# Performance work log

Hardware: AMD Instinct MI355X
Metric: run time of the kernel (lower is better)

The kernel has to match this reference:

```python
import jax, jax.numpy as jnp
import numpy as np

B, NV = 8, 2048
HALF_ANGLE = 20.0  # degrees
EXPDEL = 4.0


def to_circle(x):
    # cast angle (rad) to [-pi, pi)
    return jnp.remainder(x + jnp.pi, 2.0 * jnp.pi) - jnp.pi


def setup_inputs() -> dict:
    key = jax.random.key(0)
    k1, k2 = jax.random.split(key)
    raw = jax.random.normal(k1, (B, NV, 5), dtype=jnp.float32)
    # per-feature scaling: x, y ~ 200 m spread; v ~ N(10, 8) m/s; psi ~ N(0, pi); psidot small
    scale = jnp.array([200.0, 200.0, 8.0, np.pi, 0.1], dtype=jnp.float32)
    offset = jnp.array([0.0, 0.0, 10.0, 0.0, 0.0], dtype=jnp.float32)
    state = (raw * scale + offset).reshape(B, NV * 5)
    lengths = 4.0 + 2.0 * jax.random.uniform(k2, (NV,), dtype=jnp.float32)
    return {
        "state": state,
        "lengths": lengths,
        "v0": jnp.array([11.17], dtype=jnp.float32),
        "s0": jnp.array([3.0], dtype=jnp.float32),
        "dth": jnp.array([5.0], dtype=jnp.float32),
        "amax": jnp.array([1.5], dtype=jnp.float32),
        "b": jnp.array([4.0], dtype=jnp.float32),
    }


def reference(state, lengths, v0, s0, dth, amax, b):
    lead_dims = state.shape[:-1]
    s = state.reshape(lead_dims + (-1, 5))
    nv = s.shape[-2]
    x, y, v, psi = s[..., 0], s[..., 1], s[..., 2], s[..., 3]  # [..., nv]

    # pairwise: axis -2 = candidate i, axis -1 = ego j  (dx[i, j] = x_i - x_j)
    dx = x[..., :, None] - x[..., None, :]
    dy = y[..., :, None] - y[..., None, :]
    dr = jnp.sqrt(dx * dx + dy * dy)
    delpsi = to_circle(jnp.arctan2(dy, dx) - psi[..., None, :])  # bearing of i rel. to ego j heading
    ndist = dr * jnp.cos(delpsi)  # longitudinal distance along ego heading

    cone = (ndist > 0) & (jnp.abs(delpsi) < HALF_ANGLE * jnp.pi / 180.0)
    ndist_ = jnp.where(cone, ndist, jnp.inf)
    cndist = jnp.min(ndist_, axis=-2)       # [..., nv] nearest in-cone distance per ego
    inds = jnp.argmin(ndist_, axis=-2)      # [..., nv] index of leading vehicle

    vx = v * jnp.cos(psi)
    vy = v * jnp.sin(psi)
    dvx = jnp.take_along_axis(vx, inds, axis=-1) - vx
    dvy = jnp.take_along_axis(vy, inds, axis=-1) - vy
    dv = jnp.sqrt(dvx * dvx + dvy * dvy)
    vdelpsi = to_circle(jnp.arctan2(dvy, dvx) - psi)
    ndv = dv * jnp.cos(vdelpsi)

    sstar = s0 + v * dth + v * ndv / (2.0 * jnp.sqrt(amax * b))
    sal = cndist - lengths  # ego length subtracted (as in source)
    finite = jnp.isfinite(sal)
    sal_safe = jnp.where(finite, sal, 1.0)  # avoids inf in discarded branch

    action_free = amax * (1.0 - (v / v0) ** EXPDEL)
    action_int = -amax * (sstar / sal_safe) ** 2
    action = jnp.where(finite, action_free + action_int, action_free)
    return action[..., None]  # [..., nv, 1] to match torch output shape
```

## Files before the change

### kernel.cpp

```cpp
#include <hip/hip_runtime.h>
#include <math.h>

namespace {
constexpr int NVEH = 2048;
constexpr int THREADS = 256;
constexpr int EGOS_PER_WAVE = 4;
constexpr int WAVES = THREADS / 64;
constexpr int EGOS_PER_BLOCK = WAVES * EGOS_PER_WAVE;
constexpr int BLOCKS_PER_BATCH = NVEH / EGOS_PER_BLOCK;
}

__global__ __launch_bounds__(THREADS, 4) void idm_kernel(
    const float* __restrict__ state,
    const float* __restrict__ lengths,
    const float* __restrict__ v0p, const float* __restrict__ s0p,
    const float* __restrict__ dthp, const float* __restrict__ amaxp,
    const float* __restrict__ bp,
    float* __restrict__ out)
{
    __shared__ float2 sxy[NVEH];

    const int b = blockIdx.x / BLOCKS_PER_BATCH;
    const int egoBase = (blockIdx.x % BLOCKS_PER_BATCH) * EGOS_PER_BLOCK;
    const float* __restrict__ st = state + (size_t)b * NVEH * 5;

    for (int i = threadIdx.x; i < NVEH; i += THREADS) {
        sxy[i] = make_float2(st[i * 5 + 0], st[i * 5 + 1]);
    }
    __syncthreads();

    const int wave = threadIdx.x >> 6;
    const int lane = threadIdx.x & 63;
    const int j0 = egoBase + wave * EGOS_PER_WAVE;

    float xj[EGOS_PER_WAVE], yj[EGOS_PER_WAVE], vj[EGOS_PER_WAVE];
    float cp[EGOS_PER_WAVE], sp[EGOS_PER_WAVE];
    #pragma unroll
    for (int e = 0; e < EGOS_PER_WAVE; e++) {
        const int j = j0 + e;
        xj[e] = st[j * 5 + 0];
        yj[e] = st[j * 5 + 1];
        vj[e] = st[j * 5 + 2];
        float psi = st[j * 5 + 3];
        float s, c;
        sincosf(psi, &s, &c);
        cp[e] = c; sp[e] = s;
    }

    const float chalf = 0.93969262078590838f;
    const float c2 = chalf * chalf;

    float minv[EGOS_PER_WAVE];
    int   mini[EGOS_PER_WAVE];
    #pragma unroll
    for (int e = 0; e < EGOS_PER_WAVE; e++) { minv[e] = INFINITY; mini[e] = 0; }

    for (int k = 0; k < NVEH / 64; k++) {
        const int i = k * 64 + lane;
        const float2 xy = sxy[i];
        #pragma unroll
        for (int e = 0; e < EGOS_PER_WAVE; e++) {
            const float dx = xy.x - xj[e];
            const float dy = xy.y - yj[e];
            const float proj = dx * cp[e] + dy * sp[e];
            const float dr2 = dx * dx + dy * dy;
            const bool cone = (proj > 0.0f) && (proj * proj > dr2 * c2);
            if (cone && (proj < minv[e])) {
                minv[e] = proj;
                mini[e] = i;
            }
        }
    }

    #pragma unroll
    for (int e = 0; e < EGOS_PER_WAVE; e++) {
        float v = minv[e];
        int idx = mini[e];
        #pragma unroll
        for (int off = 32; off > 0; off >>= 1) {
            const float ov = __shfl_xor(v, off, 64);
            const int oi = __shfl_xor(idx, off, 64);
            if (ov < v || (ov == v && oi < idx)) { v = ov; idx = oi; }
        }
        minv[e] = v;
        mini[e] = idx;
    }

    if (lane == 0) {
        const float v0v = *v0p;
        const float s0v = *s0p;
        const float dthv = *dthp;
        const float am = *amaxp;
        const float bv = *bp;
        const float inv2sab = 1.0f / (2.0f * sqrtf(am * bv));

        #pragma unroll
        for (int e = 0; e < EGOS_PER_WAVE; e++) {
            const int j = j0 + e;
            const float vE = vj[e];
            const float t = vE / v0v;
            const float t2 = t * t;
            const float action_free = am * (1.0f - t2 * t2);
            float action = action_free;

            const float cnd = minv[e];
            if (cnd < 1.0e30f) {
                const int ind = mini[e];
                const float vl = st[ind * 5 + 2];
                const float pl = st[ind * 5 + 3];
                float sl, cl;
                sincosf(pl, &sl, &cl);
                const float dvx = vl * cl - vE * cp[e];
                const float dvy = vl * sl - vE * sp[e];
                const float ndv = dvx * cp[e] + dvy * sp[e];
                const float sstar = s0v + vE * dthv + vE * ndv * inv2sab;
                const float sal = cnd - lengths[j];
                const float r = sstar / sal;
                action = action_free - am * r * r;
            }
            out[b * NVEH + j] = action;
        }
    }
}

extern "C" void kernel_launch(void* const* d_in, const int* in_sizes, int n_in,
                              void* d_out, int out_size, void* d_ws, size_t ws_size,
                              hipStream_t stream) {
    const float* state   = (const float*)d_in[0];
    const float* lengths = (const float*)d_in[1];
    const float* v0      = (const float*)d_in[2];
    const float* s0      = (const float*)d_in[3];
    const float* dth     = (const float*)d_in[4];
    const float* amax    = (const float*)d_in[5];
    const float* bb      = (const float*)d_in[6];
    float* out = (float*)d_out;

    const int B = in_sizes[0] / (NVEH * 5);
    dim3 grid(B * BLOCKS_PER_BATCH);
    idm_kernel<<<grid, THREADS, 0, stream>>>(state, lengths, v0, s0, dth, amax, bb, out);
}
```

Baseline: 88.24 us.

## Pack candidate pairs into float4 LDS and vectorize cone test with packed math

Each shared-memory entry now holds two candidates (i and i+HALF), which halves LDS loads and lets the inner loop run on 2-wide float vectors that can map to packed FP32 instructions. Egos per wave rise from 4 to 8 for more register reuse, with launch bounds relaxed to 2 blocks. Ego data and sincos are computed once per lane and broadcast with shuffles, and the final epilogue runs in parallel across 8 lanes instead of serially in lane 0. The cost is higher register pressure and half as many blocks, which may lower occupancy.

```diff
diff --git a/kernel.cpp b/kernel.cpp
--- a/kernel.cpp
+++ b/kernel.cpp
@@ -1,16 +1,20 @@
 #include <hip/hip_runtime.h>
 #include <math.h>
 
+typedef float v2f __attribute__((ext_vector_type(2)));
+
 namespace {
 constexpr int NVEH = 2048;
+constexpr int HALF = NVEH / 2;
 constexpr int THREADS = 256;
-constexpr int EGOS_PER_WAVE = 4;
 constexpr int WAVES = THREADS / 64;
+constexpr int EGOS_PER_WAVE = 8;
 constexpr int EGOS_PER_BLOCK = WAVES * EGOS_PER_WAVE;
 constexpr int BLOCKS_PER_BATCH = NVEH / EGOS_PER_BLOCK;
+constexpr int ITERS = HALF / 64;
 }
 
-__global__ __launch_bounds__(THREADS, 4) void idm_kernel(
+__global__ __launch_bounds__(THREADS, 2) void idm_kernel(
     const float* __restrict__ state,
     const float* __restrict__ lengths,
     const float* __restrict__ v0p, const float* __restrict__ s0p,
@@ -18,14 +22,15 @@
     const float* __restrict__ bp,
     float* __restrict__ out)
 {
-    __shared__ float2 sxy[NVEH];
+    __shared__ float4 sxy[HALF];
 
     const int b = blockIdx.x / BLOCKS_PER_BATCH;
     const int egoBase = (blockIdx.x % BLOCKS_PER_BATCH) * EGOS_PER_BLOCK;
     const float* __restrict__ st = state + (size_t)b * NVEH * 5;
 
-    for (int i = threadIdx.x; i < NVEH; i += THREADS) {
-        sxy[i] = make_float2(st[i * 5 + 0], st[i * 5 + 1]);
+    for (int i = threadIdx.x; i < HALF; i += THREADS) {
+        sxy[i] = make_float4(st[i * 5 + 0], st[i * 5 + 1],
+                             st[(i + HALF) * 5 + 0], st[(i + HALF) * 5 + 1]);
     }
     __syncthreads();
 
@@ -33,18 +38,23 @@
     const int lane = threadIdx.x & 63;
     const int j0 = egoBase + wave * EGOS_PER_WAVE;
 
-    float xj[EGOS_PER_WAVE], yj[EGOS_PER_WAVE], vj[EGOS_PER_WAVE];
-    float cp[EGOS_PER_WAVE], sp[EGOS_PER_WAVE];
+    float ex, ey, ev, ec, es;
+    {
+        const int j = j0 + (lane & 7);
+        ex = st[j * 5 + 0];
+        ey = st[j * 5 + 1];
+        ev = st[j * 5 + 2];
+        const float ps = st[j * 5 + 3];
+        sincosf(ps, &es, &ec);
+    }
+
+    float xj[EGOS_PER_WAVE], yj[EGOS_PER_WAVE], cp[EGOS_PER_WAVE], sp[EGOS_PER_WAVE];
     #pragma unroll
     for (int e = 0; e < EGOS_PER_WAVE; e++) {
-        const int j = j0 + e;
-        xj[e] = st[j * 5 + 0];
-        yj[e] = st[j * 5 + 1];
-        vj[e] = st[j * 5 + 2];
-        float psi = st[j * 5 + 3];
-        float s, c;
-        sincosf(psi, &s, &c);
-        cp[e] = c; sp[e] = s;
+        xj[e] = __shfl(ex, e, 64);
+        yj[e] = __shfl(ey, e, 64);
+        cp[e] = __shfl(ec, e, 64);
+        sp[e] = __shfl(es, e, 64);
     }
 
     const float chalf = 0.93969262078590838f;
@@ -55,19 +65,23 @@
     #pragma unroll
     for (int e = 0; e < EGOS_PER_WAVE; e++) { minv[e] = INFINITY; mini[e] = 0; }
 
-    for (int k = 0; k < NVEH / 64; k++) {
-        const int i = k * 64 + lane;
-        const float2 xy = sxy[i];
+    for (int k = 0; k < ITERS; k++) {
+        const int i0 = k * 64 + lane;
+        const float4 c = sxy[i0];
+        const v2f xi = {c.x, c.z};
+        const v2f yi = {c.y, c.w};
         #pragma unroll
         for (int e = 0; e < EGOS_PER_WAVE; e++) {
-            const float dx = xy.x - xj[e];
-            const float dy = xy.y - yj[e];
-            const float proj = dx * cp[e] + dy * sp[e];
-            const float dr2 = dx * dx + dy * dy;
-            const bool cone = (proj > 0.0f) && (proj * proj > dr2 * c2);
-            if (cone && (proj < minv[e])) {
-                minv[e] = proj;
-                mini[e] = i;
+            const v2f dx = xi - xj[e];
+            const v2f dy = yi - yj[e];
+            const v2f proj = dx * cp[e] + dy * sp[e];
+            const v2f dr2 = dx * dx + dy * dy;
+            const v2f q = proj * proj - dr2 * c2;
+            if (proj.x > 0.0f && q.x > 0.0f && proj.x < minv[e]) {
+                minv[e] = proj.x; mini[e] = i0;
+            }
+            if (proj.y > 0.0f && q.y > 0.0f && proj.y < minv[e]) {
+                minv[e] = proj.y; mini[e] = i0 + HALF;
             }
         }
     }
@@ -86,40 +100,40 @@
         mini[e] = idx;
     }
 
-    if (lane == 0) {
+    float cnd = minv[0];
+    int ind = mini[0];
+    #pragma unroll
+    for (int e = 1; e < EGOS_PER_WAVE; e++) {
+        if ((lane & 7) == e) { cnd = minv[e]; ind = mini[e]; }
+    }
+
+    if (lane < EGOS_PER_WAVE) {
+        const int j = j0 + lane;
         const float v0v = *v0p;
         const float s0v = *s0p;
         const float dthv = *dthp;
         const float am = *amaxp;
         const float bv = *bp;
-        const float inv2sab = 1.0f / (2.0f * sqrtf(am * bv));
 
-        #pragma unroll
-        for (int e = 0; e < EGOS_PER_WAVE; e++) {
-            const int j = j0 + e;
-            const float vE = vj[e];
-            const float t = vE / v0v;
-            const float t2 = t * t;
-            const float action_free = am * (1.0f - t2 * t2);
-            float action = action_free;
+        const float t = ev / v0v;
+        const float t2 = t * t;
+        const float action_free = am * (1.0f - t2 * t2);
+        float action = action_free;
 
-            const float cnd = minv[e];
-            if (cnd < 1.0e30f) {
-                const int ind = mini[e];
-                const float vl = st[ind * 5 + 2];
-                const float pl = st[ind * 5 + 3];
-                float sl, cl;
-                sincosf(pl, &sl, &cl);
-                const float dvx = vl * cl - vE * cp[e];
-                const float dvy = vl * sl - vE * sp[e];
-                const float ndv = dvx * cp[e] + dvy * sp[e];
-                const float sstar = s0v + vE * dthv + vE * ndv * inv2sab;
-                const float sal = cnd - lengths[j];
-                const float r = sstar / sal;
-                action = action_free - am * r * r;
-            }
-            out[b * NVEH + j] = action;
+        if (cnd < 1.0e30f) {
+            const float vl = st[ind * 5 + 2];
+            const float pl = st[ind * 5 + 3];
+            float sl, cl;
+            sincosf(pl, &sl, &cl);
+            const float dvx = vl * cl - ev * ec;
+            const float dvy = vl * sl - ev * es;
+            const float ndv = dvx * ec + dvy * es;
+            const float sstar = s0v + ev * dthv + ev * ndv / (2.0f * sqrtf(am * bv));
+            const float sal = cnd - lengths[j];
+            const float r = sstar / sal;
+            action = action_free - am * r * r;
         }
+        out[b * NVEH + j] = action;
     }
 }
 
```

Measured after the change: 82.16 us. 6.9% less time.
